# Performance work log

Measured on AMD Instinct MI355X. Metric: run time of the kernel, lower is better.

The kernel has to match this reference:

```python
import jax, jax.numpy as jnp
import numpy as np

H, DQS, DQP, DVS, DVP = 12, 16, 4, 16, 8
S_SCALAR = (3.0 * DQS) ** -0.5
S_POINT = (3.0 * DQP * (9.0 * 2.0 ** 0.5)) ** -0.5
S_PAIR = 3.0 ** -0.5
_OFF = np.cumsum([0, H * DQS, H * DQS, H * DVS, H * DQP * 3, H * DQP * 3, H * DVP * 3])


def _ln(x, g, b, eps=1e-5):
    mu = x.mean(-1, keepdims=True)
    var = x.var(-1, keepdims=True)
    return (x - mu) / jnp.sqrt(var + eps) * g + b


def setup_inputs() -> dict:
    B, N, D, PD = 2, 512, 384, 128
    key = jax.random.key(0)
    ks = jax.random.split(key, 12)
    node_feats = jax.random.normal(ks[0], (B, N, D), jnp.float32)
    pair_feats = jax.random.normal(ks[1], (B, N, N, PD), jnp.float32)
    mask = jnp.ones((B, N), dtype=bool)
    # random per-residue rigid frames (orthonormal rotations via QR)
    rot = jnp.linalg.qr(jax.random.normal(ks[2], (B, N, 3, 3), jnp.float32))[0]
    trans = jax.random.normal(ks[3], (B, N, 3), jnp.float32)
    dim_qkv = int(_OFF[-1])             # 1152
    dim_out = H * (PD + DVS + 4 * DVP)  # 2112
    s = 0.02
    p = dict(
        ln_s_g=jnp.ones((D,)), ln_s_b=jnp.zeros((D,)),
        ln_p_g=jnp.ones((PD,)), ln_p_b=jnp.zeros((PD,)),
        w_pair_bias=s * jax.random.normal(ks[4], (PD, H), jnp.float32),
        w_qkv=s * jax.random.normal(ks[5], (D, dim_qkv), jnp.float32),
        point_weights=jnp.full((1, H, 1, 1), float(np.log(np.e - 1.0)), jnp.float32),
        w_out=s * jax.random.normal(ks[6], (dim_out, D), jnp.float32),
        b_out=jnp.zeros((D,)),
        ln_t_g=jnp.ones((D,)), ln_t_b=jnp.zeros((D,)),
        w_ff1=s * jax.random.normal(ks[7], (D, 4 * D), jnp.float32),
        b_ff1=jnp.zeros((4 * D,)),
        w_ff2=s * jax.random.normal(ks[8], (4 * D, D), jnp.float32),
        b_ff2=jnp.zeros((D,)),
    )
    return dict(node_feats=node_feats, pair_feats=pair_feats, mask=mask,
                rot=rot, trans=trans, **p)


def reference(node_feats, pair_feats, mask, rot, trans,
              ln_s_g, ln_s_b, ln_p_g, ln_p_b, w_pair_bias, w_qkv,
              point_weights, w_out, b_out,
              ln_t_g, ln_t_b, w_ff1, b_ff1, w_ff2, b_ff2):
    b, n, d = node_feats.shape
    x = _ln(node_feats, ln_s_g, ln_s_b)
    p = _ln(pair_feats, ln_p_g, ln_p_b)
    pair_bias = jnp.einsum('bijd,dh->bhij', p, w_pair_bias)
    qkv = x @ w_qkv  # (b,n,1152)

    def heads(t, dh):
        return t.reshape(b, n, H, dh).transpose(0, 2, 1, 3)  # b h n d

    q_s = heads(qkv[..., _OFF[0]:_OFF[1]], DQS)
    k_s = heads(qkv[..., _OFF[1]:_OFF[2]], DQS)
    v_s = heads(qkv[..., _OFF[2]:_OFF[3]], DVS)

    def to_pts(t, dp):
        pts = t.reshape(b, n, H * dp, 3)
        # rigid apply: R_i @ x + t_i (global frame)
        pts = jnp.einsum('bnxy,bnpy->bnpx', rot, pts) + trans[:, :, None, :]
        return pts.reshape(b, n, H, dp, 3).transpose(0, 2, 1, 3, 4)  # b h n d 3

    q_p = to_pts(qkv[..., _OFF[3]:_OFF[4]], DQP)
    k_p = to_pts(qkv[..., _OFF[4]:_OFF[5]], DQP)
    v_p = to_pts(qkv[..., _OFF[5]:_OFF[6]], DVP)

    scalar_logits = jnp.einsum('bhid,bhjd->bhij', q_s, k_s)
    # dist attn: -sum_{d,c} (q-k)^2, expanded to avoid (b,h,n,n,d,3) intermediate
    qq = jnp.sum(q_p * q_p, axis=(-1, -2))
    kk = jnp.sum(k_p * k_p, axis=(-1, -2))
    qk = jnp.einsum('bhidc,bhjdc->bhij', q_p, k_p)
    point_logits = -(qq[..., :, None] + kk[..., None, :] - 2.0 * qk)
    point_logits = point_logits * jax.nn.softplus(point_weights)

    neg = jnp.finfo(node_feats.dtype).min
    pm = mask[:, None, :, None] & mask[:, None, None, :]  # b 1 i j
    scalar_logits = jnp.where(pm, scalar_logits, neg)
    point_logits = jnp.where(pm, point_logits, neg)
    pair_bias = jnp.where(pm, pair_bias, neg)

    logits = S_SCALAR * scalar_logits + S_POINT * point_logits + S_PAIR * pair_bias
    attn = jax.nn.softmax(logits, axis=-1)

    out_s = jnp.einsum('bhij,bhjd->bhid', attn, v_s)
    out_pair = jnp.einsum('bhij,bijd->bhid', attn, p)
    out_p = jnp.einsum('bhij,bhjdc->bhidc', attn, v_p)
    # rigid inverse: R_i^T (x - t_i) back to local frame
    pts = out_p.transpose(0, 2, 1, 3, 4).reshape(b, n, H * DVP, 3)
    pts = jnp.einsum('bnyx,bnpy->bnpx', rot, pts - trans[:, :, None, :])
    out_p = pts.reshape(b, n, H, DVP, 3)
    pnorm = jnp.sqrt(jnp.sum(out_p * out_p, axis=-1) + 1e-8)  # safe_norm

    cat = jnp.concatenate([
        out_s.transpose(0, 2, 1, 3).reshape(b, n, H * DVS),
        out_p.reshape(b, n, H * DVP * 3),
        pnorm.reshape(b, n, H * DVP),
        out_pair.transpose(0, 2, 1, 3).reshape(b, n, -1),
    ], axis=-1)
    attn_out = cat @ w_out + b_out

    # residuals + transition (dropout=0 -> identity). Note: transition is
    # applied to attn_out (pre-residual), exactly as in the torch forward.
    node1 = attn_out + node_feats
    t = _ln(attn_out, ln_t_g, ln_t_b)
    t = jax.nn.gelu(t @ w_ff1 + b_ff1) @ w_ff2 + b_ff2
    return t + node1
```

## Files before the change

### kernel.cpp

```cpp
#include <hip/hip_runtime.h>
#include <hip/hip_bf16.h>
#include <math.h>

typedef __hip_bfloat16 bf16;
typedef _Float16 f16;
typedef unsigned short ushort_t;
typedef ushort_t ushort8 __attribute__((ext_vector_type(8)));
typedef ushort_t us4 __attribute__((ext_vector_type(4)));
typedef short bf16x8 __attribute__((ext_vector_type(8)));
typedef f16 f16x8 __attribute__((ext_vector_type(8)));
typedef float f32x4 __attribute__((ext_vector_type(4)));

constexpr float S_SCALAR = 0.14433756729740643f;
constexpr float S_POINT  = 0.08091531528f;
constexpr float S_PAIR   = 0.5773502691896258f;

__device__ inline short f2bfs(float x) {
  return (short)__builtin_bit_cast(unsigned short, __float2bfloat16(x));
}
__device__ inline ushort_t f2bfu(float x) {
  return (ushort_t)__builtin_bit_cast(unsigned short, __float2bfloat16(x));
}
__device__ inline ushort_t f2hu(float x) {
  return __builtin_bit_cast(ushort_t, (f16)x);
}
__device__ inline float h2f(ushort_t u) {
  return (float)__builtin_bit_cast(f16, u);
}

__device__ inline float gelu_tanh(float x) {
  float c = 0.7978845608028654f * (x + 0.044715f * x * x * x);
  return 0.5f * x * (1.f + tanhf(c));
}

__global__ __launch_bounds__(128) void ln384_kernel(
    const float* __restrict__ in, const float* __restrict__ g,
    const float* __restrict__ b, float* __restrict__ out)
{
  int row = blockIdx.x;
  const float* x = in + (size_t)row * 384;
  int t = threadIdx.x;
  float v[3]; float s = 0.f, s2 = 0.f;
#pragma unroll
  for (int i = 0; i < 3; i++) { v[i] = x[t + 128 * i]; s += v[i]; s2 += v[i] * v[i]; }
  for (int o = 32; o; o >>= 1) { s += __shfl_down(s, o); s2 += __shfl_down(s2, o); }
  __shared__ float sh[4];
  int wid = t >> 6, lane = t & 63;
  if (lane == 0) { sh[wid] = s; sh[2 + wid] = s2; }
  __syncthreads();
  s = sh[0] + sh[1]; s2 = sh[2] + sh[3];
  float mean = s * (1.f / 384.f);
  float var = s2 * (1.f / 384.f) - mean * mean;
  float rstd = rsqrtf(fmaxf(var, 0.f) + 1e-5f);
  float* orow = out + (size_t)row * 384;
#pragma unroll
  for (int i = 0; i < 3; i++) {
    int c = t + 128 * i;
    orow[c] = (v[i] - mean) * rstd * g[c] + b[c];
  }
}

__global__ __launch_bounds__(256) void prep_all_kernel(
    const float* __restrict__ w_qkv, const float* __restrict__ w_out,
    const float* __restrict__ w_ff1, const float* __restrict__ w_ff2,
    ushort_t* __restrict__ wqkvT, ushort_t* __restrict__ woutT,
    ushort_t* __restrict__ wff1T, ushort_t* __restrict__ wff2T,
    const float* __restrict__ g, const float* __restrict__ bb,
    const float* __restrict__ wpb, ushort_t* __restrict__ gwbT,
    float* __restrict__ gsbs,
    const float* __restrict__ node, const float* __restrict__ ln_s_g,
    const float* __restrict__ ln_s_b, float* __restrict__ xout)
{
  __shared__ float shmem[2048];
  int bid = blockIdx.x;
  int t = threadIdx.x;
  if (bid < 2376) {
    const float* src; ushort_t* dst; int K, N, bx, by;
    if (bid < 432)       { src = w_qkv; dst = wqkvT; K = 384;  N = 1152; bx = bid % 36;          by = bid / 36; }
    else if (bid < 1224) { src = w_out; dst = woutT; K = 2112; N = 384;  bx = (bid - 432) % 12;  by = (bid - 432) / 12; }
    else if (bid < 1800) { src = w_ff1; dst = wff1T; K = 384;  N = 1536; bx = (bid - 1224) % 48; by = (bid - 1224) / 48; }
    else                 { src = w_ff2; dst = wff2T; K = 1536; N = 384;  bx = (bid - 1800) % 12; by = (bid - 1800) / 12; }
    float (&tile)[32][33] = *reinterpret_cast<float (*)[32][33]>(shmem);
    int n0 = bx * 32, k0 = by * 32;
    int c = t & 31, r4 = (t >> 5) * 4;
#pragma unroll
    for (int i = 0; i < 4; i++)
      tile[r4 + i][c] = src[(size_t)(k0 + r4 + i) * N + n0 + c];
    __syncthreads();
#pragma unroll
    for (int i = 0; i < 4; i++)
      dst[(size_t)(n0 + r4 + i) * K + k0 + c] = f2bfu(tile[c][r4 + i]);
    return;
  }
  if (bid == 2376) {
    for (int idx = t; idx < 2048; idx += 256) {
      int h = idx >> 7, c = idx & 127;
      float v = (h < 12) ? g[c] * wpb[c * 12 + h] : 0.f;
      bf16 r = __float2bfloat16(v);
      gwbT[idx] = __builtin_bit_cast(unsigned short, r);
      shmem[idx] = __bfloat162float(r);
    }
    __syncthreads();
    if (t < 16) {
      float s = 0.f;
      for (int c = 0; c < 128; c++) s += shmem[t * 128 + c];
      gsbs[t] = s;
    } else if (t < 32) {
      int h = t - 16;
      float s = 0.f;
      if (h < 12) for (int c = 0; c < 128; c++) s = fmaf(bb[c], wpb[c * 12 + h], s);
      gsbs[t] = s;
    }
    return;
  }
  int half = t >> 7, tt = t & 127;
  int row = (bid - 2377) * 2 + half;
  const float* x = node + (size_t)row * 384;
  float v[3]; float s = 0.f, s2 = 0.f;
#pragma unroll
  for (int i = 0; i < 3; i++) { v[i] = x[tt + 128 * i]; s += v[i]; s2 += v[i] * v[i]; }
  for (int o = 32; o; o >>= 1) { s += __shfl_down(s, o); s2 += __shfl_down(s2, o); }
  int wid = t >> 6, lane = t & 63;
  if (lane == 0) { shmem[wid] = s; shmem[4 + wid] = s2; }
  __syncthreads();
  s = shmem[half * 2] + shmem[half * 2 + 1];
  s2 = shmem[4 + half * 2] + shmem[4 + half * 2 + 1];
  float mean = s * (1.f / 384.f);
  float var = s2 * (1.f / 384.f) - mean * mean;
  float rstd = rsqrtf(fmaxf(var, 0.f) + 1e-5f);
  float* orow = xout + (size_t)row * 384;
#pragma unroll
  for (int i = 0; i < 3; i++) {
    int c = tt + 128 * i;
    orow[c] = (v[i] - mean) * rstd * ln_s_g[c] + ln_s_b[c];
  }
}

template <int EPI>
__global__ __launch_bounds__(256) void gemm_mfma_kernel(
    const float* __restrict__ A, const ushort_t* __restrict__ BT,
    const float* __restrict__ bias, const float* __restrict__ r1,
    const float* __restrict__ r2, float* __restrict__ C,
    int M, int Nn, int K)
{
  __shared__ ushort_t As[64][72];
  __shared__ ushort_t Bs[64][72];
  int t = threadIdx.x;
  int w = t >> 6, l = t & 63;
  int m0 = blockIdx.y * 64, n0 = blockIdx.x * 64;
  int wm = (w >> 1) * 32, wn = (w & 1) * 32;
  int lr = l & 15, lk = l >> 4;
  int sr = t >> 2, sc = (t & 3) * 16;
  f32x4 acc[2][2];
#pragma unroll
  for (int i = 0; i < 2; i++)
#pragma unroll
    for (int j = 0; j < 2; j++) acc[i][j] = (f32x4){0.f, 0.f, 0.f, 0.f};

  for (int k0 = 0; k0 < K; k0 += 64) {
    const float* Ar = A + (size_t)(m0 + sr) * K + k0 + sc;
    const ushort_t* Br = BT + (size_t)(n0 + sr) * K + k0 + sc;
    float4 a0 = *(const float4*)(Ar + 0);
    float4 a1 = *(const float4*)(Ar + 4);
    float4 a2 = *(const float4*)(Ar + 8);
    float4 a3 = *(const float4*)(Ar + 12);
    ushort8 b0 = *(const ushort8*)(Br + 0);
    ushort8 b1 = *(const ushort8*)(Br + 8);
    ushort8 u0, u1;
    u0[0] = f2bfu(a0.x); u0[1] = f2bfu(a0.y); u0[2] = f2bfu(a0.z); u0[3] = f2bfu(a0.w);
    u0[4] = f2bfu(a1.x); u0[5] = f2bfu(a1.y); u0[6] = f2bfu(a1.z); u0[7] = f2bfu(a1.w);
    u1[0] = f2bfu(a2.x); u1[1] = f2bfu(a2.y); u1[2] = f2bfu(a2.z); u1[3] = f2bfu(a2.w);
    u1[4] = f2bfu(a3.x); u1[5] = f2bfu(a3.y); u1[6] = f2bfu(a3.z); u1[7] = f2bfu(a3.w);
    *(ushort8*)&As[sr][sc] = u0;
    *(ushort8*)&As[sr][sc + 8] = u1;
    *(ushort8*)&Bs[sr][sc] = b0;
    *(ushort8*)&Bs[sr][sc + 8] = b1;
    __syncthreads();
#pragma unroll
    for (int kk = 0; kk < 2; kk++) {
      bf16x8 af0 = *(const bf16x8*)&As[wm + lr][kk * 32 + lk * 8];
      bf16x8 af1 = *(const bf16x8*)&As[wm + 16 + lr][kk * 32 + lk * 8];
      bf16x8 bf0 = *(const bf16x8*)&Bs[wn + lr][kk * 32 + lk * 8];
      bf16x8 bf1 = *(const bf16x8*)&Bs[wn + 16 + lr][kk * 32 + lk * 8];
      acc[0][0] = __builtin_amdgcn_mfma_f32_16x16x32_bf16(af0, bf0, acc[0][0], 0, 0, 0);
      acc[0][1] = __builtin_amdgcn_mfma_f32_16x16x32_bf16(af0, bf1, acc[0][1], 0, 0, 0);
      acc[1][0] = __builtin_amdgcn_mfma_f32_16x16x32_bf16(af1, bf0, acc[1][0], 0, 0, 0);
      acc[1][1] = __builtin_amdgcn_mfma_f32_16x16x32_bf16(af1, bf1, acc[1][1], 0, 0, 0);
    }
    __syncthreads();
  }
#pragma unroll
  for (int mf = 0; mf < 2; mf++) {
#pragma unroll
    for (int nf = 0; nf < 2; nf++) {
      int nn = n0 + wn + nf * 16 + lr;
      float bv = bias ? bias[nn] : 0.f;
#pragma unroll
      for (int e = 0; e < 4; e++) {
        int m = m0 + wm + mf * 16 + lk * 4 + e;
        float v = acc[mf][nf][e] + bv;
        if (EPI == 1) v = gelu_tanh(v);
        if (EPI == 2) v += r1[(size_t)m * Nn + nn] + r2[(size_t)m * Nn + nn];
        C[(size_t)m * Nn + nn] = v;
      }
    }
  }
}

template <int EPI>
__global__ __launch_bounds__(256) void gemm_mfma_m32_kernel(
    const float* __restrict__ A, const ushort_t* __restrict__ BT,
    const float* __restrict__ bias, const float* __restrict__ r1,
    const float* __restrict__ r2, float* __restrict__ C,
    int M, int Nn, int K)
{
  __shared__ ushort_t As[32][72];
  __shared__ ushort_t Bs[64][72];
  int t = threadIdx.x;
  int w = t >> 6, l = t & 63;
  int m0 = blockIdx.y * 32, n0 = blockIdx.x * 64;
  int wm = (w & 1) * 16, wn = (w >> 1) * 32;
  int lr = l & 15, lk = l >> 4;
  int ar = t >> 3, ac = (t & 7) * 8;
  int br = t >> 2, bc = (t & 3) * 16;
  f32x4 acc[2];
  acc[0] = (f32x4){0.f, 0.f, 0.f, 0.f};
  acc[1] = (f32x4){0.f, 0.f, 0.f, 0.f};

  for (int k0 = 0; k0 < K; k0 += 64) {
    const float* Ar = A + (size_t)(m0 + ar) * K + k0 + ac;
    float4 a0 = *(const float4*)(Ar + 0);
    float4 a1 = *(const float4*)(Ar + 4);
    ushort8 u;
    u[0] = f2bfu(a0.x); u[1] = f2bfu(a0.y); u[2] = f2bfu(a0.z); u[3] = f2bfu(a0.w);
    u[4] = f2bfu(a1.x); u[5] = f2bfu(a1.y); u[6] = f2bfu(a1.z); u[7] = f2bfu(a1.w);
    *(ushort8*)&As[ar][ac] = u;
    const ushort_t* Br = BT + (size_t)(n0 + br) * K + k0 + bc;
    *(ushort8*)&Bs[br][bc] = *(const ushort8*)(Br + 0);
    *(ushort8*)&Bs[br][bc + 8] = *(const ushort8*)(Br + 8);
    __syncthreads();
#pragma unroll
    for (int kk = 0; kk < 2; kk++) {
      bf16x8 af = *(const bf16x8*)&As[wm + lr][kk * 32 + lk * 8];
      bf16x8 bf0 = *(const bf16x8*)&Bs[wn + lr][kk * 32 + lk * 8];
      bf16x8 bf1 = *(const bf16x8*)&Bs[wn + 16 + lr][kk * 32 + lk * 8];
      acc[0] = __builtin_amdgcn_mfma_f32_16x16x32_bf16(af, bf0, acc[0], 0, 0, 0);
      acc[1] = __builtin_amdgcn_mfma_f32_16x16x32_bf16(af, bf1, acc[1], 0, 0, 0);
    }
    __syncthreads();
  }
#pragma unroll
  for (int nf = 0; nf < 2; nf++) {
    int nn = n0 + wn + nf * 16 + lr;
    float bv = bias ? bias[nn] : 0.f;
#pragma unroll
    for (int e = 0; e < 4; e++) {
      int m = m0 + wm + lk * 4 + e;
      float v = acc[nf][e] + bv;
      if (EPI == 1) v = gelu_tanh(v);
      if (EPI == 2) v += r1[(size_t)m * Nn + nn] + r2[(size_t)m * Nn + nn];
      C[(size_t)m * Nn + nn] = v;
    }
  }
}

__global__ __launch_bounds__(256) void qkv_post_kernel(
    const float* __restrict__ qkv, const float* __restrict__ rot,
    const float* __restrict__ trans, const float* __restrict__ pw,
    f16* __restrict__ qhat, f16* __restrict__ khat,
    float* __restrict__ kkb, ushort_t* __restrict__ vT)
{
  int bh = blockIdx.x;
  int b = bh / 12, h = bh - b * 12;
  int role = blockIdx.y >> 1;
  int j = (blockIdx.y & 1) * 256 + threadIdx.x;
  int bn = b * 512 + j;
  const float* row = qkv + (size_t)bn * 1152;
  float R[9];
#pragma unroll
  for (int k = 0; k < 9; k++) R[k] = rot[bn * 9 + k];
  float T0 = trans[bn * 3], T1 = trans[bn * 3 + 1], T2 = trans[bn * 3 + 2];
  if (role == 0) {
    float sp = log1pf(__expf(pw[h]));
    float c1 = 2.f * S_POINT * sp;
    f16* qh = qhat + ((size_t)bh * 512 + j) * 32;
#pragma unroll
    for (int d = 0; d < 16; d++) qh[d] = (f16)(S_SCALAR * row[h * 16 + d]);
#pragma unroll
    for (int p = 0; p < 4; p++) {
      int base = 576 + (h * 4 + p) * 3;
      float x = row[base], y = row[base + 1], z = row[base + 2];
      qh[16 + p * 3 + 0] = (f16)(c1 * (R[0] * x + R[1] * y + R[2] * z + T0));
      qh[16 + p * 3 + 1] = (f16)(c1 * (R[3] * x + R[4] * y + R[5] * z + T1));
      qh[16 + p * 3 + 2] = (f16)(c1 * (R[6] * x + R[7] * y + R[8] * z + T2));
    }
#pragma unroll
    for (int d = 28; d < 32; d++) qh[d] = (f16)0.f;
  } else if (role == 1) {
    f16* kh = khat + ((size_t)bh * 512 + j) * 32;
#pragma unroll
    for (int d = 0; d < 16; d++) kh[d] = (f16)(row[192 + h * 16 + d]);
    float kksum = 0.f;
#pragma unroll
    for (int p = 0; p < 4; p++) {
      int base = 720 + (h * 4 + p) * 3;
      float x = row[base], y = row[base + 1], z = row[base + 2];
      float gx = R[0] * x + R[1] * y + R[2] * z + T0;
      float gy = R[3] * x + R[4] * y + R[5] * z + T1;
      float gz = R[6] * x + R[7] * y + R[8] * z + T2;
      kh[16 + p * 3 + 0] = (f16)gx; kh[16 + p * 3 + 1] = (f16)gy; kh[16 + p * 3 + 2] = (f16)gz;
      kksum = fmaf(gx, gx, kksum); kksum = fmaf(gy, gy, kksum); kksum = fmaf(gz, gz, kksum);
    }
#pragma unroll
    for (int d = 28; d < 32; d++) kh[d] = (f16)0.f;
    kkb[(size_t)bh * 512 + j] = kksum;
  } else {
    ushort_t* vt = vT + (size_t)bh * 40 * 512;
#pragma unroll
    for (int c = 0; c < 16; c++) vt[c * 512 + j] = f2hu(row[384 + h * 16 + c]);
#pragma unroll
    for (int p = 0; p < 8; p++) {
      int base = 864 + (h * 8 + p) * 3;
      float x = row[base], y = row[base + 1], z = row[base + 2];
      vt[(16 + p * 3 + 0) * 512 + j] = f2hu(R[0] * x + R[1] * y + R[2] * z + T0);
      vt[(16 + p * 3 + 1) * 512 + j] = f2hu(R[3] * x + R[4] * y + R[5] * z + T1);
      vt[(16 + p * 3 + 2) * 512 + j] = f2hu(R[6] * x + R[7] * y + R[8] * z + T2);
    }
  }
}

__global__ __launch_bounds__(256) void pair_bias_kernel(
    const float* __restrict__ pair, const ushort_t* __restrict__ gwbT,
    const float* __restrict__ gsbs, const float* __restrict__ g,
    const float* __restrict__ bb, ushort_t* __restrict__ bias,
    f16* __restrict__ pnT)
{
  __shared__ ushort_t tile[128][136];
  int t = threadIdx.x;
  int wv = t >> 6, l = t & 63;
  int lr = l & 15, lk = l >> 4;
  size_t rid0 = (size_t)blockIdx.x * 128 + (size_t)wv * 32;

  bf16x8 bfrag[4];
#pragma unroll
  for (int kc = 0; kc < 4; kc++) {
    const ushort_t* gp = gwbT + lr * 128 + kc * 32 + lk * 8;
    us4 q0 = *(const us4*)gp;
    us4 q1 = *(const us4*)(gp + 4);
    bfrag[kc][0] = (short)q0[0]; bfrag[kc][1] = (short)q0[1];
    bfrag[kc][2] = (short)q0[2]; bfrag[kc][3] = (short)q0[3];
    bfrag[kc][4] = (short)q1[0]; bfrag[kc][5] = (short)q1[1];
    bfrag[kc][6] = (short)q1[2]; bfrag[kc][7] = (short)q1[3];
  }

  const float* p0 = pair + (rid0 + lr) * 128 + lk * 8;
  f32x4 acc0 = {0.f, 0.f, 0.f, 0.f}, acc1 = {0.f, 0.f, 0.f, 0.f};
  float s0 = 0.f, s20 = 0.f, s1 = 0.f, s21 = 0.f;
#pragma unroll
  for (int kc = 0; kc < 4; kc++) {
    float4 u0 = *(const float4*)(p0 + kc * 32);
    float4 u1 = *(const float4*)(p0 + kc * 32 + 4);
    float4 w0 = *(const float4*)(p0 + 2048 + kc * 32);
    float4 w1 = *(const float4*)(p0 + 2048 + kc * 32 + 4);
    s0 += u0.x + u0.y + u0.z + u0.w + u1.x + u1.y + u1.z + u1.w;
    s20 = fmaf(u0.x, u0.x, s20); s20 = fmaf(u0.y, u0.y, s20);
    s20 = fmaf(u0.z, u0.z, s20); s20 = fmaf(u0.w, u0.w, s20);
    s20 = fmaf(u1.x, u1.x, s20); s20 = fmaf(u1.y, u1.y, s20);
    s20 = fmaf(u1.z, u1.z, s20); s20 = fmaf(u1.w, u1.w, s20);
    s1 += w0.x + w0.y + w0.z + w0.w + w1.x + w1.y + w1.z + w1.w;
    s21 = fmaf(w0.x, w0.x, s21); s21 = fmaf(w0.y, w0.y, s21);
    s21 = fmaf(w0.z, w0.z, s21); s21 = fmaf(w0.w, w0.w, s21);
    s21 = fmaf(w1.x, w1.x, s21); s21 = fmaf(w1.y, w1.y, s21);
    s21 = fmaf(w1.z, w1.z, s21); s21 = fmaf(w1.w, w1.w, s21);
    bf16x8 a0, a1;
    a0[0] = f2bfs(u0.x); a0[1] = f2bfs(u0.y); a0[2] = f2bfs(u0.z); a0[3] = f2bfs(u0.w);
    a0[4] = f2bfs(u1.x); a0[5] = f2bfs(u1.y); a0[6] = f2bfs(u1.z); a0[7] = f2bfs(u1.w);
    a1[0] = f2bfs(w0.x); a1[1] = f2bfs(w0.y); a1[2] = f2bfs(w0.z); a1[3] = f2bfs(w0.w);
    a1[4] = f2bfs(w1.x); a1[5] = f2bfs(w1.y); a1[6] = f2bfs(w1.z); a1[7] = f2bfs(w1.w);
    acc0 = __builtin_amdgcn_mfma_f32_16x16x32_bf16(a0, bfrag[kc], acc0, 0, 0, 0);
    acc1 = __builtin_amdgcn_mfma_f32_16x16x32_bf16(a1, bfrag[kc], acc1, 0, 0, 0);
  }
  s0 += __shfl_xor(s0, 16);  s0 += __shfl_xor(s0, 32);
  s20 += __shfl_xor(s20, 16); s20 += __shfl_xor(s20, 32);
  s1 += __shfl_xor(s1, 16);  s1 += __shfl_xor(s1, 32);
  s21 += __shfl_xor(s21, 16); s21 += __shfl_xor(s21, 32);
  float mean0 = s0 * (1.f / 128.f);
  float rstd0 = rsqrtf(fmaxf(s20 * (1.f / 128.f) - mean0 * mean0, 0.f) + 1e-5f);
  float mean1 = s1 * (1.f / 128.f);
  float rstd1 = rsqrtf(fmaxf(s21 * (1.f / 128.f) - mean1 * mean1, 0.f) + 1e-5f);

  int jl_u = wv * 32 + lr, jl_w = wv * 32 + 16 + lr;
#pragma unroll
  for (int kc = 0; kc < 4; kc++) {
    int c0 = kc * 32 + lk * 8;
    float4 u0 = *(const float4*)(p0 + kc * 32);
    float4 u1 = *(const float4*)(p0 + kc * 32 + 4);
    float4 w0 = *(const float4*)(p0 + 2048 + kc * 32);
    float4 w1 = *(const float4*)(p0 + 2048 + kc * 32 + 4);
    float4 g0 = *(const float4*)(g + c0);
    float4 g1 = *(const float4*)(g + c0 + 4);
    float4 b0 = *(const float4*)(bb + c0);
    float4 b1 = *(const float4*)(bb + c0 + 4);
    float uu[8] = {u0.x, u0.y, u0.z, u0.w, u1.x, u1.y, u1.z, u1.w};
    float ww[8] = {w0.x, w0.y, w0.z, w0.w, w1.x, w1.y, w1.z, w1.w};
    float gg[8] = {g0.x, g0.y, g0.z, g0.w, g1.x, g1.y, g1.z, g1.w};
    float bv[8] = {b0.x, b0.y, b0.z, b0.w, b1.x, b1.y, b1.z, b1.w};
#pragma unroll
    for (int e = 0; e < 8; e++) {
      int c = c0 + e;
      int sw = ((c >> 3) & 7) << 4;
      tile[c][jl_u ^ sw] = f2hu(fmaf((uu[e] - mean0) * rstd0, gg[e], bv[e]));
      tile[c][jl_w ^ sw] = f2hu(fmaf((ww[e] - mean1) * rstd1, gg[e], bv[e]));
    }
  }
  __syncthreads();
  {
    int slab = blockIdx.x >> 2;
    int j0blk = (blockIdx.x & 3) * 128;
    ushort_t* dstb = (ushort_t*)pnT + (size_t)slab * 65536 + j0blk;
#pragma unroll
    for (int it = 0; it < 8; it++) {
      int idx = t + 256 * it;
      int c = idx >> 4, o = idx & 15;
      int sw = ((c >> 3) & 7) << 4;
      ushort8 v = *(const ushort8*)&tile[c][(o * 8) ^ sw];
      *(ushort8*)(dstb + (size_t)c * 512 + o * 8) = v;
    }
  }

  float gsum = gsbs[lr], bsum = gsbs[16 + lr];
  int b = (int)(rid0 >> 18);
  int i = (int)((rid0 >> 9) & 511);
  int j0 = (int)(rid0 & 511);
  us4 pk0, pk1;
#pragma unroll
  for (int e = 0; e < 4; e++) {
    int r = lk * 4 + e;
    float m0 = __shfl(mean0, r), rs0 = __shfl(rstd0, r);
    float m1 = __shfl(mean1, r), rs1 = __shfl(rstd1, r);
    pk0[e] = f2hu(rs0 * (acc0[e] - m0 * gsum) + bsum);
    pk1[e] = f2hu(rs1 * (acc1[e] - m1 * gsum) + bsum);
  }
  if (lr < 12) {
    ushort_t* dst = bias + ((size_t)(b * 12 + lr) * 512 + i) * 512 + j0 + lk * 4;
    *(us4*)dst = pk0;
    *(us4*)(dst + 16) = pk1;
  }
}

__global__ __launch_bounds__(256, 1) void attn_kernel(
    const f16* __restrict__ qhat, const f16* __restrict__ khat,
    const float* __restrict__ kkb, const ushort_t* __restrict__ bias,
    const float* __restrict__ pw, ushort_t* __restrict__ attn)
{
  int i0 = blockIdx.x * 64;
  int bh = blockIdx.y;
  int b = bh / 12, h = bh - b * 12;
  int t = threadIdx.x;
  int w = t >> 6, l = t & 63, lr = l & 15, lk = l >> 4;
  float spp = S_POINT * log1pf(__expf(pw[h]));
  int i = i0 + w * 16 + lr;
  f16x8 bfrag = *(const f16x8*)(qhat + ((size_t)bh * 512 + i) * 32 + lk * 8);
  const f16* kbase = khat + (size_t)bh * 512 * 32;
  const float* kkrow = kkb + (size_t)bh * 512;
  const ushort_t* brow = bias + ((size_t)bh * 512 + i) * 512;
  float lg[32][4];
  float pmax = -3.0e38f;
#pragma unroll
  for (int jt = 0; jt < 32; jt++) {
    f16x8 afrag = *(const f16x8*)(kbase + (size_t)(jt * 16 + lr) * 32 + lk * 8);
    f32x4 c = {0.f, 0.f, 0.f, 0.f};
    c = __builtin_amdgcn_mfma_f32_16x16x32_f16(afrag, bfrag, c, 0, 0, 0);
    us4 bq = *(const us4*)(brow + jt * 16 + lk * 4);
    float4 kq = *(const float4*)(kkrow + jt * 16 + lk * 4);
    float kk4[4] = {kq.x, kq.y, kq.z, kq.w};
#pragma unroll
    for (int e = 0; e < 4; e++) {
      float lv = c[e] + S_PAIR * h2f(bq[e]) - spp * kk4[e];
      lg[jt][e] = lv;
      pmax = fmaxf(pmax, lv);
    }
  }
  pmax = fmaxf(pmax, __shfl_xor(pmax, 16));
  pmax = fmaxf(pmax, __shfl_xor(pmax, 32));
  float ssum = 0.f;
#pragma unroll
  for (int jt = 0; jt < 32; jt++)
#pragma unroll
    for (int e = 0; e < 4; e++) {
      float p = __expf(lg[jt][e] - pmax);
      lg[jt][e] = p;
      ssum += p;
    }
  ssum += __shfl_xor(ssum, 16);
  ssum += __shfl_xor(ssum, 32);
  float inv = 1.f / ssum;
  ushort_t* arow = attn + ((size_t)(b * 512 + i) * 12 + h) * 512;
#pragma unroll
  for (int jt = 0; jt < 32; jt++) {
    us4 o;
#pragma unroll
    for (int e = 0; e < 4; e++) o[e] = f2hu(lg[jt][e] * inv);
    *(us4*)(arow + jt * 16 + lk * 4) = o;
  }
}

__global__ __launch_bounds__(256) void sv_gemm_kernel(
    const ushort_t* __restrict__ attn, const ushort_t* __restrict__ vT,
    float* __restrict__ svraw)
{
  int i0 = blockIdx.x * 64;
  int bh = blockIdx.y;
  int b = bh / 12, h = bh - b * 12;
  __shared__ ushort_t As_[64][72];
  __shared__ ushort_t Bs_[48][72];
  int t = threadIdx.x;
  int w = t >> 6, l = t & 63, lr = l & 15, lk = l >> 4;
  int ai = t >> 2, as = (t & 3) * 16;
  const ushort_t* vbase = vT + (size_t)bh * 40 * 512;
  f32x4 acc[3];
#pragma unroll
  for (int n = 0; n < 3; n++) acc[n] = (f32x4){0.f, 0.f, 0.f, 0.f};

  for (int jt = 0; jt < 8; jt++) {
    int jb = jt * 64;
    size_t aoff = ((size_t)(b * 512 + i0 + ai) * 12 + h) * 512 + jb + as;
    ushort8 a0 = *(const ushort8*)(attn + aoff);
    ushort8 a1 = *(const ushort8*)(attn + aoff + 8);
    *(ushort8*)&As_[ai][as] = a0;
    *(ushort8*)&As_[ai][as + 8] = a1;
    for (int idx = t; idx < 384; idx += 256) {
      int c = idx >> 3, j8 = (idx & 7) * 8;
      ushort8 v = {0, 0, 0, 0, 0, 0, 0, 0};
      if (c < 40) v = *(const ushort8*)(vbase + (size_t)c * 512 + jb + j8);
      *(ushort8*)&Bs_[c][j8] = v;
    }
    __syncthreads();
#pragma unroll
    for (int kk = 0; kk < 2; kk++) {
      f16x8 af = *(const f16x8*)&As_[w * 16 + lr][kk * 32 + lk * 8];
#pragma unroll
      for (int n = 0; n < 3; n++) {
        f16x8 bf_ = *(const f16x8*)&Bs_[n * 16 + lr][kk * 32 + lk * 8];
        acc[n] = __builtin_amdgcn_mfma_f32_16x16x32_f16(af, bf_, acc[n], 0, 0, 0);
      }
    }
    __syncthreads();
  }
#pragma unroll
  for (int n = 0; n < 3; n++) {
    int c = n * 16 + lr;
    if (c < 40) {
#pragma unroll
      for (int e = 0; e < 4; e++) {
        int i = i0 + w * 16 + lk * 4 + e;
        svraw[(size_t)(b * 512 + i) * 480 + h * 40 + c] = acc[n][e];
      }
    }
  }
}

__global__ __launch_bounds__(256) void pair_out_kernel(
    const ushort_t* __restrict__ attn, const f16* __restrict__ pnT,
    const float* __restrict__ svraw, const float* __restrict__ rot,
    const float* __restrict__ trans, float* __restrict__ cat)
{
  int bn = blockIdx.x;
  int t = threadIdx.x;
  const float* sv = svraw + (size_t)bn * 480;
  float* crow = cat + (size_t)bn * 2112;
  if (t < 192) {
    int h2 = t >> 4, d = t & 15;
    crow[t] = sv[h2 * 40 + d];
    if (t < 96) {
      int h3 = t >> 3, dp = t & 7;
      float T0 = trans[bn * 3], T1 = trans[bn * 3 + 1], T2 = trans[bn * 3 + 2];
      const float* R = rot + bn * 9;
      float px = sv[h3 * 40 + 16 + dp * 3 + 0] - T0;
      float py = sv[h3 * 40 + 16 + dp * 3 + 1] - T1;
      float pz = sv[h3 * 40 + 16 + dp * 3 + 2] - T2;
      float lx = R[0] * px + R[3] * py + R[6] * pz;
      float ly = R[1] * px + R[4] * py + R[7] * pz;
      float lz = R[2] * px + R[5] * py + R[8] * pz;
      crow[192 + h3 * 24 + dp * 3 + 0] = lx;
      crow[192 + h3 * 24 + dp * 3 + 1] = ly;
      crow[192 + h3 * 24 + dp * 3 + 2] = lz;
      crow[480 + h3 * 8 + dp] = sqrtf(lx * lx + ly * ly + lz * lz + 1e-8f);
    }
  }
  int w = t >> 6, l = t & 63, lr = l & 15, lk = l >> 4;
  const ushort_t* arow = attn + (size_t)bn * 12 * 512;
  int ar = (lr < 12) ? lr : 11;
  const f16* slab = pnT + (size_t)bn * 65536;
  int n0 = w * 32;
  f32x4 acc0 = {0.f, 0.f, 0.f, 0.f}, acc1 = {0.f, 0.f, 0.f, 0.f};
#pragma unroll
  for (int ks = 0; ks < 16; ks++) {
    int kb = ks * 32 + lk * 8;
    f16x8 af = *(const f16x8*)((const f16*)arow + (size_t)ar * 512 + kb);
    f16x8 b0 = *(const f16x8*)(slab + (size_t)(n0 + lr) * 512 + kb);
    f16x8 b1 = *(const f16x8*)(slab + (size_t)(n0 + 16 + lr) * 512 + kb);
    acc0 = __builtin_amdgcn_mfma_f32_16x16x32_f16(af, b0, acc0, 0, 0, 0);
    acc1 = __builtin_amdgcn_mfma_f32_16x16x32_f16(af, b1, acc1, 0, 0, 0);
  }
#pragma unroll
  for (int e = 0; e < 4; e++) {
    int hh = lk * 4 + e;
    if (hh < 12) {
      crow[576 + hh * 128 + n0 + lr] = acc0[e];
      crow[576 + hh * 128 + n0 + 16 + lr] = acc1[e];
    }
  }
}

extern "C" void kernel_launch(void* const* d_in, const int* in_sizes, int n_in,
                              void* d_out, int out_size, void* d_ws, size_t ws_size,
                              hipStream_t stream)
{
  const float* node   = (const float*)d_in[0];
  const float* pair   = (const float*)d_in[1];
  const float* rot    = (const float*)d_in[3];
  const float* trans  = (const float*)d_in[4];
  const float* ln_s_g = (const float*)d_in[5];
  const float* ln_s_b = (const float*)d_in[6];
  const float* ln_p_g = (const float*)d_in[7];
  const float* ln_p_b = (const float*)d_in[8];
  const float* wpb    = (const float*)d_in[9];
  const float* w_qkv  = (const float*)d_in[10];
  const float* pw     = (const float*)d_in[11];
  const float* w_out  = (const float*)d_in[12];
  const float* b_out  = (const float*)d_in[13];
  const float* ln_t_g = (const float*)d_in[14];
  const float* ln_t_b = (const float*)d_in[15];
  const float* w_ff1  = (const float*)d_in[16];
  const float* b_ff1  = (const float*)d_in[17];
  const float* w_ff2  = (const float*)d_in[18];
  const float* b_ff2  = (const float*)d_in[19];
  float* out = (float*)d_out;
  float* ws = (float*)d_ws;

  float* qkv    = ws;
  float* x      = ws + 1179648;
  float* tn     = x;
  float* ao     = ws + 1572864;
  float* svraw  = ws + 1966080;
  ushort_t* biasb = (ushort_t*)(ws + 2457600);
  float* cat    = ws + 2457600;
  ushort_t* attnb = (ushort_t*)(ws + 5603328);
  float* gb     = ws + 5603328;
  ushort_t* gwbT = (ushort_t*)(ws + 8749056);
  float* gsbs   = ws + 8750080;
  ushort_t* wqkvT = (ushort_t*)(ws + 8750112);
  ushort_t* woutT = (ushort_t*)(ws + 8971296);
  ushort_t* wff1T = (ushort_t*)(ws + 9376800);
  ushort_t* wff2T = (ushort_t*)(ws + 9671712);
  f16* qhat     = (f16*)(ws + 9966624);
  f16* khat     = (f16*)(ws + 10163232);
  float* kkb    = ws + 10359840;
  ushort_t* vT  = (ushort_t*)(ws + 10372128);
  f16* pnT      = (f16*)(ws + 10617888);

  prep_all_kernel<<<2889, 256, 0, stream>>>(w_qkv, w_out, w_ff1, w_ff2,
      wqkvT, woutT, wff1T, wff2T, ln_p_g, ln_p_b, wpb, gwbT, gsbs,
      node, ln_s_g, ln_s_b, x);
  gemm_mfma_kernel<0><<<dim3(18, 16), 256, 0, stream>>>(x, wqkvT, nullptr, nullptr, nullptr, qkv, 1024, 1152, 384);
  qkv_post_kernel<<<dim3(24, 6), 256, 0, stream>>>(qkv, rot, trans, pw, qhat, khat, kkb, vT);
  pair_bias_kernel<<<4096, 256, 0, stream>>>(pair, gwbT, gsbs, ln_p_g, ln_p_b, biasb, pnT);
  attn_kernel<<<dim3(8, 24), 256, 0, stream>>>(qhat, khat, kkb, biasb, pw, attnb);
  sv_gemm_kernel<<<dim3(8, 24), 256, 0, stream>>>(attnb, vT, svraw);
  pair_out_kernel<<<1024, 256, 0, stream>>>(attnb, pnT, svraw, rot, trans, cat);
  gemm_mfma_m32_kernel<0><<<dim3(6, 32), 256, 0, stream>>>(cat, woutT, b_out, nullptr, nullptr, ao, 1024, 384, 2112);
  ln384_kernel<<<1024, 128, 0, stream>>>(ao, ln_t_g, ln_t_b, tn);
  gemm_mfma_kernel<1><<<dim3(24, 16), 256, 0, stream>>>(tn, wff1T, b_ff1, nullptr, nullptr, gb, 1024, 1536, 384);
  gemm_mfma_m32_kernel<2><<<dim3(6, 32), 256, 0, stream>>>(gb, wff2T, b_ff2, ao, node, out, 1024, 384, 1536);
}
```

Before: 587.6 us.

## Recompute pair layernorm in pair_out instead of materializing transposed pnT

pair_bias_kernel now stores only per-row mean and rstd instead of writing a normalized, transposed f16 copy of pair features. pair_out_kernel rereads the fp32 pair tensor, applies the layernorm on the fly, transposes through a swizzled LDS tile, and feeds MFMA. This removes one large write pass and its intermediate buffer. In exchange it doubles the fp32 reads of pair and adds LDS staging and syncs inside pair_out.

```diff
diff --git a/kernel.cpp b/kernel.cpp
--- a/kernel.cpp
+++ b/kernel.cpp
@@ -331,11 +331,9 @@
 
 __global__ __launch_bounds__(256) void pair_bias_kernel(
     const float* __restrict__ pair, const ushort_t* __restrict__ gwbT,
-    const float* __restrict__ gsbs, const float* __restrict__ g,
-    const float* __restrict__ bb, ushort_t* __restrict__ bias,
-    f16* __restrict__ pnT)
-{
-  __shared__ ushort_t tile[128][136];
+    const float* __restrict__ gsbs, ushort_t* __restrict__ bias,
+    float* __restrict__ meanb, float* __restrict__ rstdb)
+{
   int t = threadIdx.x;
   int wv = t >> 6, l = t & 63;
   int lr = l & 15, lk = l >> 4;
@@ -388,46 +386,10 @@
   float rstd0 = rsqrtf(fmaxf(s20 * (1.f / 128.f) - mean0 * mean0, 0.f) + 1e-5f);
   float mean1 = s1 * (1.f / 128.f);
   float rstd1 = rsqrtf(fmaxf(s21 * (1.f / 128.f) - mean1 * mean1, 0.f) + 1e-5f);
-
-  int jl_u = wv * 32 + lr, jl_w = wv * 32 + 16 + lr;
-#pragma unroll
-  for (int kc = 0; kc < 4; kc++) {
-    int c0 = kc * 32 + lk * 8;
-    float4 u0 = *(const float4*)(p0 + kc * 32);
-    float4 u1 = *(const float4*)(p0 + kc * 32 + 4);
-    float4 w0 = *(const float4*)(p0 + 2048 + kc * 32);
-    float4 w1 = *(const float4*)(p0 + 2048 + kc * 32 + 4);
-    float4 g0 = *(const float4*)(g + c0);
-    float4 g1 = *(const float4*)(g + c0 + 4);
-    float4 b0 = *(const float4*)(bb + c0);
-    float4 b1 = *(const float4*)(bb + c0 + 4);
-    float uu[8] = {u0.x, u0.y, u0.z, u0.w, u1.x, u1.y, u1.z, u1.w};
-    float ww[8] = {w0.x, w0.y, w0.z, w0.w, w1.x, w1.y, w1.z, w1.w};
-    float gg[8] = {g0.x, g0.y, g0.z, g0.w, g1.x, g1.y, g1.z, g1.w};
-    float bv[8] = {b0.x, b0.y, b0.z, b0.w, b1.x, b1.y, b1.z, b1.w};
-#pragma unroll
-    for (int e = 0; e < 8; e++) {
-      int c = c0 + e;
-      int sw = ((c >> 3) & 7) << 4;
-      tile[c][jl_u ^ sw] = f2hu(fmaf((uu[e] - mean0) * rstd0, gg[e], bv[e]));
-      tile[c][jl_w ^ sw] = f2hu(fmaf((ww[e] - mean1) * rstd1, gg[e], bv[e]));
-    }
-  }
-  __syncthreads();
-  {
-    int slab = blockIdx.x >> 2;
-    int j0blk = (blockIdx.x & 3) * 128;
-    ushort_t* dstb = (ushort_t*)pnT + (size_t)slab * 65536 + j0blk;
-#pragma unroll
-    for (int it = 0; it < 8; it++) {
-      int idx = t + 256 * it;
-      int c = idx >> 4, o = idx & 15;
-      int sw = ((c >> 3) & 7) << 4;
-      ushort8 v = *(const ushort8*)&tile[c][(o * 8) ^ sw];
-      *(ushort8*)(dstb + (size_t)c * 512 + o * 8) = v;
-    }
-  }
-
+  if (lk == 0) {
+    meanb[rid0 + lr] = mean0;      rstdb[rid0 + lr] = rstd0;
+    meanb[rid0 + 16 + lr] = mean1; rstdb[rid0 + 16 + lr] = rstd1;
+  }
   float gsum = gsbs[lr], bsum = gsbs[16 + lr];
   int b = (int)(rid0 >> 18);
   int i = (int)((rid0 >> 9) & 511);
@@ -561,7 +523,9 @@
 }
 
 __global__ __launch_bounds__(256) void pair_out_kernel(
-    const ushort_t* __restrict__ attn, const f16* __restrict__ pnT,
+    const ushort_t* __restrict__ attn, const float* __restrict__ pair,
+    const float* __restrict__ meanb, const float* __restrict__ rstdb,
+    const float* __restrict__ g, const float* __restrict__ bb,
     const float* __restrict__ svraw, const float* __restrict__ rot,
     const float* __restrict__ trans, float* __restrict__ cat)
 {
@@ -588,20 +552,50 @@
       crow[480 + h3 * 8 + dp] = sqrtf(lx * lx + ly * ly + lz * lz + 1e-8f);
     }
   }
+  __shared__ ushort_t tile[128][136];
+  __shared__ float rsL[512], nmuL[512];
+  __shared__ float gl[128], bl[128];
+  if (t < 128) { gl[t] = g[t]; bl[t] = bb[t]; }
+  for (int j = t; j < 512; j += 256) {
+    float rs = rstdb[(size_t)bn * 512 + j];
+    rsL[j] = rs;
+    nmuL[j] = -meanb[(size_t)bn * 512 + j] * rs;
+  }
   int w = t >> 6, l = t & 63, lr = l & 15, lk = l >> 4;
   const ushort_t* arow = attn + (size_t)bn * 12 * 512;
   int ar = (lr < 12) ? lr : 11;
-  const f16* slab = pnT + (size_t)bn * 65536;
   int n0 = w * 32;
+  int sw0 = (((n0 + lr) >> 3) & 7) << 4;
+  int sw1 = (((n0 + 16 + lr) >> 3) & 7) << 4;
   f32x4 acc0 = {0.f, 0.f, 0.f, 0.f}, acc1 = {0.f, 0.f, 0.f, 0.f};
-#pragma unroll
-  for (int ks = 0; ks < 16; ks++) {
-    int kb = ks * 32 + lk * 8;
-    f16x8 af = *(const f16x8*)((const f16*)arow + (size_t)ar * 512 + kb);
-    f16x8 b0 = *(const f16x8*)(slab + (size_t)(n0 + lr) * 512 + kb);
-    f16x8 b1 = *(const f16x8*)(slab + (size_t)(n0 + 16 + lr) * 512 + kb);
-    acc0 = __builtin_amdgcn_mfma_f32_16x16x32_f16(af, b0, acc0, 0, 0, 0);
-    acc1 = __builtin_amdgcn_mfma_f32_16x16x32_f16(af, b1, acc1, 0, 0, 0);
+  int jl = t & 127, ch = (t >> 7) * 64;
+  for (int jt = 0; jt < 4; jt++) {
+    __syncthreads();
+    int jg = jt * 128 + jl;
+    float rs = rsL[jg], nmu = nmuL[jg];
+    const float4* prow = (const float4*)(pair + ((size_t)bn * 512 + jg) * 128 + ch);
+#pragma unroll
+    for (int q = 0; q < 16; q++) {
+      float4 v = prow[q];
+      int c = ch + q * 4;
+      int sw = ((c >> 3) & 7) << 4;
+      int jj = jl ^ sw;
+      tile[c + 0][jj] = f2hu(fmaf(fmaf(v.x, rs, nmu), gl[c + 0], bl[c + 0]));
+      tile[c + 1][jj] = f2hu(fmaf(fmaf(v.y, rs, nmu), gl[c + 1], bl[c + 1]));
+      tile[c + 2][jj] = f2hu(fmaf(fmaf(v.z, rs, nmu), gl[c + 2], bl[c + 2]));
+      tile[c + 3][jj] = f2hu(fmaf(fmaf(v.w, rs, nmu), gl[c + 3], bl[c + 3]));
+    }
+    __syncthreads();
+#pragma unroll
+    for (int ks = 0; ks < 4; ks++) {
+      int kb = jt * 128 + ks * 32 + lk * 8;
+      int kl = ks * 32 + lk * 8;
+      f16x8 af = *(const f16x8*)((const f16*)arow + (size_t)ar * 512 + kb);
+      f16x8 b0 = *(const f16x8*)&tile[n0 + lr][kl ^ sw0];
+      f16x8 b1 = *(const f16x8*)&tile[n0 + 16 + lr][kl ^ sw1];
+      acc0 = __builtin_amdgcn_mfma_f32_16x16x32_f16(af, b0, acc0, 0, 0, 0);
+      acc1 = __builtin_amdgcn_mfma_f32_16x16x32_f16(af, b1, acc1, 0, 0, 0);
+    }
   }
 #pragma unroll
   for (int e = 0; e < 4; e++) {
@@ -658,17 +652,18 @@
   f16* khat     = (f16*)(ws + 10163232);
   float* kkb    = ws + 10359840;
   ushort_t* vT  = (ushort_t*)(ws + 10372128);
-  f16* pnT      = (f16*)(ws + 10617888);
+  float* meanb  = ws + 10617888;
+  float* rstdb  = ws + 11142176;
 
   prep_all_kernel<<<2889, 256, 0, stream>>>(w_qkv, w_out, w_ff1, w_ff2,
       wqkvT, woutT, wff1T, wff2T, ln_p_g, ln_p_b, wpb, gwbT, gsbs,
       node, ln_s_g, ln_s_b, x);
   gemm_mfma_kernel<0><<<dim3(18, 16), 256, 0, stream>>>(x, wqkvT, nullptr, nullptr, nullptr, qkv, 1024, 1152, 384);
   qkv_post_kernel<<<dim3(24, 6), 256, 0, stream>>>(qkv, rot, trans, pw, qhat, khat, kkb, vT);
-  pair_bias_kernel<<<4096, 256, 0, stream>>>(pair, gwbT, gsbs, ln_p_g, ln_p_b, biasb, pnT);
+  pair_bias_kernel<<<4096, 256, 0, stream>>>(pair, gwbT, gsbs, biasb, meanb, rstdb);
   attn_kernel<<<dim3(8, 24), 256, 0, stream>>>(qhat, khat, kkb, biasb, pw, attnb);
   sv_gemm_kernel<<<dim3(8, 24), 256, 0, stream>>>(attnb, vT, svraw);
-  pair_out_kernel<<<1024, 256, 0, stream>>>(attnb, pnT, svraw, rot, trans, cat);
+  pair_out_kernel<<<1024, 256, 0, stream>>>(attnb, pair, meanb, rstdb, ln_p_g, ln_p_b, svraw, rot, trans, cat);
   gemm_mfma_m32_kernel<0><<<dim3(6, 32), 256, 0, stream>>>(cat, woutT, b_out, nullptr, nullptr, ao, 1024, 384, 2112);
   ln384_kernel<<<1024, 128, 0, stream>>>(ao, ln_t_g, ln_t_b, tn);
   gemm_mfma_kernel<1><<<dim3(24, 16), 256, 0, stream>>>(tn, wff1T, b_ff1, nullptr, nullptr, gb, 1024, 1536, 384);
```

Result: faster. 574.3 us (-2.3%).
